# Performance work log

Hardware: AMD Instinct MI355X
Metric: run time of the kernel (lower is better)

## Reference

```python
import jax, jax.numpy as jnp
import numpy as np

T, B, I, H = 512, 64, 1024, 1024
DROPOUT = 0.3


def setup_inputs() -> dict:
    key = jax.random.key(0)
    k = jax.random.split(key, 6)
    s = 1.0 / np.sqrt(H).astype(np.float32)
    x = jax.random.normal(k[0], (T, B, I), dtype=jnp.float32)
    w_ih = jax.random.uniform(k[1], (4 * H, I), minval=-s, maxval=s, dtype=jnp.float32)
    w_hh = jax.random.uniform(k[2], (4 * H, H), minval=-s, maxval=s, dtype=jnp.float32)
    b_ih = jax.random.uniform(k[3], (4 * H,), minval=-s, maxval=s, dtype=jnp.float32)
    b_hh = jax.random.uniform(k[4], (4 * H,), minval=-s, maxval=s, dtype=jnp.float32)
    # init_weights: forget-gate bias (second quarter) set to 1
    b_ih = b_ih.at[H:2 * H].set(1.0)
    b_hh = b_hh.at[H:2 * H].set(1.0)
    # DropConnect mask on recurrent weights (training-mode dropout, fixed realization)
    keep = jax.random.bernoulli(k[5], 1.0 - DROPOUT, (4 * H, H))
    hh_mask = keep.astype(jnp.float32) / (1.0 - DROPOUT)
    return {"x": x, "w_ih": w_ih, "w_hh": w_hh, "b_ih": b_ih, "b_hh": b_hh, "hh_mask": hh_mask}


def reference(x, w_ih, w_hh, b_ih, b_hh, hh_mask):
    # x: (T, B, I). PyTorch LSTM gate order: i, f, g, o.
    h = w_hh.shape[1]
    w_hh_dropped = w_hh * hh_mask  # DropConnect applied once per forward
    # Precompute input contribution for all timesteps (one big GEMM): (T, B, 4H)
    gx = jnp.einsum('tbi,gi->tbg', x, w_ih) + b_ih + b_hh

    def step(carry, g_t):
        h_t, c_t = carry
        gates = g_t + h_t @ w_hh_dropped.T  # (B, 4H)
        i_g, f_g, g_g, o_g = jnp.split(gates, 4, axis=-1)
        i_g = jax.nn.sigmoid(i_g)
        f_g = jax.nn.sigmoid(f_g)
        g_g = jnp.tanh(g_g)
        o_g = jax.nn.sigmoid(o_g)
        c_new = f_g * c_t + i_g * g_g
        h_new = o_g * jnp.tanh(c_new)
        return (h_new, c_new), h_new

    bsz = x.shape[1]
    init = (jnp.zeros((bsz, h), x.dtype), jnp.zeros((bsz, h), x.dtype))
    (hn, cn), out = jax.lax.scan(step, init, gx)
    # match torch: output (T,B,H), hn/cn with leading num_layers dim
    return out, hn[None], cn[None]
```

## Files before the change

### kernel.cpp

```cpp
#include <hip/hip_runtime.h>

#define TT 512
#define BB 64
#define II 1024
#define HH 1024
#define GG 4096
#define BH 65536
#define NBLK 128

typedef __attribute__((ext_vector_type(8))) short bf16x8;
typedef __attribute__((ext_vector_type(4))) float f32x4;
typedef __attribute__((ext_vector_type(4))) unsigned u32x4;

__device__ __forceinline__ float bf2f(unsigned short u) {
  union { unsigned int i; float f; } v; v.i = ((unsigned int)u) << 16; return v.f;
}
__device__ __forceinline__ unsigned short f2bf(float f) {
  union { float f; unsigned int i; } v; v.f = f;
  return (unsigned short)((v.i + 0x7FFFu + ((v.i >> 16) & 1u)) >> 16);
}
__device__ __forceinline__ bf16x8 pack8(float4 a, float4 b) {
  union { bf16x8 v; unsigned short u[8]; } p;
  p.u[0] = f2bf(a.x); p.u[1] = f2bf(a.y); p.u[2] = f2bf(a.z); p.u[3] = f2bf(a.w);
  p.u[4] = f2bf(b.x); p.u[5] = f2bf(b.y); p.u[6] = f2bf(b.z); p.u[7] = f2bf(b.w);
  return p.v;
}
__device__ __forceinline__ float sigmoid_f(float x) { return 1.0f / (1.0f + __expf(-x)); }
__device__ __forceinline__ float tanh_f(float x) {
  float e = __expf(-2.0f * fabsf(x));
  float t = (1.0f - e) / (1.0f + e);
  return copysignf(t, x);
}

__device__ __forceinline__ void st32_uc(unsigned* p, unsigned v) {
  __hip_atomic_store(p, v, __ATOMIC_RELAXED, __HIP_MEMORY_SCOPE_AGENT);
}
__device__ __forceinline__ unsigned ld32_uc(const unsigned* p) {
  return __hip_atomic_load(p, __ATOMIC_RELAXED, __HIP_MEMORY_SCOPE_AGENT);
}
__device__ __forceinline__ void st128_uc(void* p, u32x4 v) {
  asm volatile("global_store_dwordx4 %0, %1, off sc0 sc1" :: "v"(p), "v"(v) : "memory");
}

__global__ __launch_bounds__(256) void wdlstm_xconv(
    const float* __restrict__ xc, unsigned short* __restrict__ xbf, int n4) {
  int stride = gridDim.x * blockDim.x;
  for (int i = blockIdx.x * blockDim.x + threadIdx.x; i < n4; i += stride) {
    float4 v = *(const float4*)(xc + (size_t)i * 4);
    unsigned short o[4] = {f2bf(v.x), f2bf(v.y), f2bf(v.z), f2bf(v.w)};
    *(unsigned long long*)(xbf + (size_t)i * 4) = *(unsigned long long*)o;
  }
}

__global__ __launch_bounds__(256) void wdlstm_fused(
    const float* __restrict__ w_hh, const float* __restrict__ hh_mask,
    const float* __restrict__ w_ih,
    const float* __restrict__ b_ih, const float* __restrict__ b_hh,
    const unsigned short* __restrict__ xbf,
    float* __restrict__ out, float* __restrict__ c_state,
    unsigned* __restrict__ flags,
    unsigned short* __restrict__ hinit,
    unsigned short* __restrict__ hring,
    int t0, int tc) {
  __shared__ __align__(16) char Wh[65536];
  __shared__ __align__(16) char Wi[65536];
  __shared__ float Dlds[64][35];
  __shared__ __align__(16) unsigned Hs[64][4];

  const int tid = threadIdx.x;
  const int wv  = tid >> 6, l = tid & 63;
  const int ln  = l & 15, lq = l >> 4;
  const int j0h = blockIdx.x * 8;
  unsigned* g_step = flags + 2048;

#pragma unroll
  for (int c8 = 0; c8 < 16; ++c8) {
    int c = tid + 256 * c8;
    int n = c >> 7, cc = c & 127;
    int wrow = (n >> 3) * HH + j0h + (n & 7);
    int addr = (n * 2048 + cc * 16) ^ ((n & 7) << 4);
    {
      const float* sw = w_hh   + (size_t)wrow * HH + cc * 8;
      const float* sm = hh_mask + (size_t)wrow * HH + cc * 8;
      float4 w0 = *(const float4*)sw, w1 = *(const float4*)(sw + 4);
      float4 m0 = *(const float4*)sm, m1 = *(const float4*)(sm + 4);
      float4 p0 = {w0.x * m0.x, w0.y * m0.y, w0.z * m0.z, w0.w * m0.w};
      float4 p1 = {w1.x * m1.x, w1.y * m1.y, w1.z * m1.z, w1.w * m1.w};
      *(bf16x8*)(Wh + addr) = pack8(p0, p1);
    }
    {
      const float* si = w_ih + (size_t)wrow * II + cc * 8;
      float4 a0 = *(const float4*)si, a1 = *(const float4*)(si + 4);
      *(bf16x8*)(Wi + addr) = pack8(a0, a1);
    }
  }
  __syncthreads();

  const int b_ep = l;
  const int jj0  = 2 * wv;
  float c_reg[2];
  if (t0 == 0) {
    c_reg[0] = c_reg[1] = 0.f;
  } else {
    float2 cv = *(const float2*)(c_state + (size_t)b_ep * HH + j0h + jj0);
    c_reg[0] = cv.x; c_reg[1] = cv.y;
  }
  float biasv[4][2];
#pragma unroll
  for (int g = 0; g < 4; ++g)
#pragma unroll
    for (int q = 0; q < 2; ++q) {
      int col = g * HH + j0h + jj0 + q;
      biasv[g][q] = b_ih[col] + b_hh[col];
    }

  float* hn_out = out + (size_t)TT * BH;
  float* cn_out = hn_out + BH;

  f32x4 gxacc[2];
  auto gx_compute = [&](int lt) {
    gxacc[0] = (f32x4){0.f, 0.f, 0.f, 0.f};
    gxacc[1] = (f32x4){0.f, 0.f, 0.f, 0.f};
    const unsigned short* ap = xbf + (size_t)lt * BH + (size_t)(16 * wv + ln) * II + lq * 8;
#pragma unroll 4
    for (int kc = 0; kc < 32; ++kc) {
      bf16x8 a = *(const bf16x8*)(ap + kc * 32);
#pragma unroll
      for (int ni = 0; ni < 2; ++ni) {
        int n = 16 * ni + ln;
        int baddr = (n * 2048 + kc * 64 + lq * 16) ^ ((n & 7) << 4);
        bf16x8 b = *(const bf16x8*)(Wi + baddr);
        gxacc[ni] = __builtin_amdgcn_mfma_f32_16x16x32_bf16(a, b, gxacc[ni], 0, 0, 0);
      }
    }
  };
  gx_compute(0);

  for (int lt = 0; lt < tc; ++lt) {
    const int t = t0 + lt;

    f32x4 acc[2] = {gxacc[0], gxacc[1]};

    if (t > 0) {
      if (blockIdx.x == 0) {
        if (tid < 64) {
          const unsigned* f0 = flags + (2 * tid) * 16;
          const unsigned* f1 = flags + (2 * tid + 1) * 16;
          while ((int)ld32_uc(f0) < t || (int)ld32_uc(f1) < t)
            __builtin_amdgcn_s_sleep(1);
          if (tid == 0) st32_uc(g_step, (unsigned)t);
        }
        __syncthreads();
      } else {
        if (tid == 0) {
          while ((int)ld32_uc(g_step) < t) __builtin_amdgcn_s_sleep(1);
        }
        __syncthreads();
      }

      const unsigned short* hp = (lt == 0) ? hinit
                                           : hring + (size_t)(lt - 1) * BH;
      const unsigned short* ap = hp + (size_t)(16 * wv + ln) * HH + lq * 8;
#pragma unroll 4
      for (int kc = 0; kc < 32; ++kc) {
        bf16x8 a = *(const bf16x8*)(ap + kc * 32);
#pragma unroll
        for (int ni = 0; ni < 2; ++ni) {
          int n = 16 * ni + ln;
          int baddr = (n * 2048 + kc * 64 + lq * 16) ^ ((n & 7) << 4);
          bf16x8 b = *(const bf16x8*)(Wh + baddr);
          acc[ni] = __builtin_amdgcn_mfma_f32_16x16x32_bf16(a, b, acc[ni], 0, 0, 0);
        }
      }
    }
#pragma unroll
    for (int ni = 0; ni < 2; ++ni)
#pragma unroll
      for (int r = 0; r < 4; ++r)
        Dlds[16 * wv + 4 * lq + r][16 * ni + ln] = acc[ni][r];
    __syncthreads();

    float hq[2];
#pragma unroll
    for (int q = 0; q < 2; ++q) {
      float g0 = Dlds[b_ep][ 0 + jj0 + q] + biasv[0][q];
      float g1 = Dlds[b_ep][ 8 + jj0 + q] + biasv[1][q];
      float g2 = Dlds[b_ep][16 + jj0 + q] + biasv[2][q];
      float g3 = Dlds[b_ep][24 + jj0 + q] + biasv[3][q];
      float ig = sigmoid_f(g0);
      float fg = sigmoid_f(g1);
      float gg = tanh_f(g2);
      float og = sigmoid_f(g3);
      c_reg[q] = fg * c_reg[q] + ig * gg;
      hq[q] = og * tanh_f(c_reg[q]);
    }
    *(float2*)(out + (size_t)t * BH + (size_t)b_ep * HH + j0h + jj0) = make_float2(hq[0], hq[1]);
    Hs[b_ep][wv] = (unsigned)f2bf(hq[0]) | ((unsigned)f2bf(hq[1]) << 16);
    if (t == TT - 1) {
      *(float2*)(hn_out + (size_t)b_ep * HH + j0h + jj0) = make_float2(hq[0], hq[1]);
      *(float2*)(cn_out + (size_t)b_ep * HH + j0h + jj0) = make_float2(c_reg[0], c_reg[1]);
    }

    __syncthreads();

    if (wv == 0) {
      u32x4 hv4 = *(const u32x4*)&Hs[l][0];
      char* dst = (char*)hring + ((size_t)lt * BH + (size_t)l * HH + j0h) * 2;
      st128_uc(dst, hv4);
      if (lt == tc - 1) {
        char* dsti = (char*)hinit + ((size_t)l * HH + j0h) * 2;
        st128_uc(dsti, hv4);
      }
      asm volatile("s_waitcnt vmcnt(0)" ::: "memory");
      if (tid == 0) st32_uc(&flags[blockIdx.x * 16], (unsigned)(t + 1));
    }

    if (lt + 1 < tc) gx_compute(lt + 1);
  }

  *(float2*)(c_state + (size_t)b_ep * HH + j0h + jj0) = make_float2(c_reg[0], c_reg[1]);
}

extern "C" void kernel_launch(void* const* d_in, const int* in_sizes, int n_in,
                              void* d_out, int out_size, void* d_ws, size_t ws_size,
                              hipStream_t stream) {
  const float* x       = (const float*)d_in[0];
  const float* w_ih    = (const float*)d_in[1];
  const float* w_hh    = (const float*)d_in[2];
  const float* b_ih    = (const float*)d_in[3];
  const float* b_hh    = (const float*)d_in[4];
  const float* hh_mask = (const float*)d_in[5];
  float* out           = (float*)d_out;

  char* ws = (char*)d_ws;
  float* c_state        = (float*)ws;
  unsigned* flags       = (unsigned*)(ws + 262144);
  unsigned short* hinit = (unsigned short*)(ws + 278528);
  unsigned short* hring = (unsigned short*)(ws + 409600);

  const long long fixed = 409600;
  const long long per_t = 131072 + 131072;
  long long avail = (long long)ws_size - fixed;
  int TC = (int)(avail / per_t);
  if (TC > 128) TC = 128;
  if (TC < 2) TC = 2;
  unsigned short* xbf = (unsigned short*)(ws + 409600 + (size_t)TC * 131072);

  hipMemsetAsync(flags, 0, 16384, stream);

  for (int t0 = 0; t0 < TT; t0 += TC) {
    int tc = TT - t0 < TC ? TT - t0 : TC;
    const float* xc = x + (size_t)t0 * BB * II;
    wdlstm_xconv<<<256, 256, 0, stream>>>(xc, xbf, tc * BH / 4);
    wdlstm_fused<<<NBLK, 256, 0, stream>>>(w_hh, hh_mask, w_ih, b_ih, b_hh, xbf,
                                           out, c_state, flags, hinit, hring, t0, tc);
  }
}
```

Baseline: 4.663 ms.

## Split recurrent K-reduction across two wave groups with 512-thread blocks

Doubles the block to 512 threads and splits each per-step GEMM's K dimension in half across two wave groups. The partial sums are reduced through a doubled LDS staging buffer, and the pointwise epilogue is reassigned so each thread owns one hidden column. All A-operand loads are also issued up front into registers before the MFMA chain, to hide global latency on the serial recurrent path. This shortens the per-step critical path, at the cost of more register pressure from the 16 preloaded vectors, an extra LDS add, and 8 waves contending for the CU.

New measurement: 4.585 ms. About the same (-1.7%).

```diff
diff --git a/kernel.cpp b/kernel.cpp
--- a/kernel.cpp
+++ b/kernel.cpp
@@ -52,7 +52,7 @@
   }
 }
 
-__global__ __launch_bounds__(256) void wdlstm_fused(
+__global__ __launch_bounds__(512) void wdlstm_fused(
     const float* __restrict__ w_hh, const float* __restrict__ hh_mask,
     const float* __restrict__ w_ih,
     const float* __restrict__ b_ih, const float* __restrict__ b_hh,
@@ -64,18 +64,20 @@
     int t0, int tc) {
   __shared__ __align__(16) char Wh[65536];
   __shared__ __align__(16) char Wi[65536];
-  __shared__ float Dlds[64][35];
-  __shared__ __align__(16) unsigned Hs[64][4];
+  __shared__ float Dlds[2][64][35];
+  __shared__ __align__(16) unsigned short Hs[64][8];
 
   const int tid = threadIdx.x;
   const int wv  = tid >> 6, l = tid & 63;
   const int ln  = l & 15, lq = l >> 4;
+  const int r0  = 16 * (wv & 3);
+  const int kh  = wv >> 2;
   const int j0h = blockIdx.x * 8;
   unsigned* g_step = flags + 2048;
 
 #pragma unroll
-  for (int c8 = 0; c8 < 16; ++c8) {
-    int c = tid + 256 * c8;
+  for (int c8 = 0; c8 < 8; ++c8) {
+    int c = tid + 512 * c8;
     int n = c >> 7, cc = c & 127;
     int wrow = (n >> 3) * HH + j0h + (n & 7);
     int addr = (n * 2048 + cc * 16) ^ ((n & 7) << 4);
@@ -96,23 +98,17 @@
   }
   __syncthreads();
 
-  const int b_ep = l;
-  const int jj0  = 2 * wv;
-  float c_reg[2];
-  if (t0 == 0) {
-    c_reg[0] = c_reg[1] = 0.f;
-  } else {
-    float2 cv = *(const float2*)(c_state + (size_t)b_ep * HH + j0h + jj0);
-    c_reg[0] = cv.x; c_reg[1] = cv.y;
-  }
-  float biasv[4][2];
-#pragma unroll
-  for (int g = 0; g < 4; ++g)
-#pragma unroll
-    for (int q = 0; q < 2; ++q) {
-      int col = g * HH + j0h + jj0 + q;
-      biasv[g][q] = b_ih[col] + b_hh[col];
-    }
+  const int b_ep = tid & 63;
+  const int jc   = tid >> 6;
+  float c_reg;
+  if (t0 == 0) c_reg = 0.f;
+  else         c_reg = c_state[(size_t)b_ep * HH + j0h + jc];
+  float biasv[4];
+#pragma unroll
+  for (int g = 0; g < 4; ++g) {
+    int col = g * HH + j0h + jc;
+    biasv[g] = b_ih[col] + b_hh[col];
+  }
 
   float* hn_out = out + (size_t)TT * BH;
   float* cn_out = hn_out + BH;
@@ -121,16 +117,19 @@
   auto gx_compute = [&](int lt) {
     gxacc[0] = (f32x4){0.f, 0.f, 0.f, 0.f};
     gxacc[1] = (f32x4){0.f, 0.f, 0.f, 0.f};
-    const unsigned short* ap = xbf + (size_t)lt * BH + (size_t)(16 * wv + ln) * II + lq * 8;
-#pragma unroll 4
-    for (int kc = 0; kc < 32; ++kc) {
-      bf16x8 a = *(const bf16x8*)(ap + kc * 32);
+    const unsigned short* ap = xbf + (size_t)lt * BH + (size_t)(r0 + ln) * II + kh * 512 + lq * 8;
+    bf16x8 areg[16];
+#pragma unroll
+    for (int i = 0; i < 16; ++i) areg[i] = *(const bf16x8*)(ap + i * 32);
+#pragma unroll
+    for (int i = 0; i < 16; ++i) {
+      int kb = kh * 1024 + i * 64;
 #pragma unroll
       for (int ni = 0; ni < 2; ++ni) {
         int n = 16 * ni + ln;
-        int baddr = (n * 2048 + kc * 64 + lq * 16) ^ ((n & 7) << 4);
+        int baddr = (n * 2048 + kb + lq * 16) ^ ((n & 7) << 4);
         bf16x8 b = *(const bf16x8*)(Wi + baddr);
-        gxacc[ni] = __builtin_amdgcn_mfma_f32_16x16x32_bf16(a, b, gxacc[ni], 0, 0, 0);
+        gxacc[ni] = __builtin_amdgcn_mfma_f32_16x16x32_bf16(areg[i], b, gxacc[ni], 0, 0, 0);
       }
     }
   };
@@ -160,16 +159,19 @@
 
       const unsigned short* hp = (lt == 0) ? hinit
                                            : hring + (size_t)(lt - 1) * BH;
-      const unsigned short* ap = hp + (size_t)(16 * wv + ln) * HH + lq * 8;
-#pragma unroll 4
-      for (int kc = 0; kc < 32; ++kc) {
-        bf16x8 a = *(const bf16x8*)(ap + kc * 32);
+      const unsigned short* ap = hp + (size_t)(r0 + ln) * HH + kh * 512 + lq * 8;
+      bf16x8 areg[16];
+#pragma unroll
+      for (int i = 0; i < 16; ++i) areg[i] = *(const bf16x8*)(ap + i * 32);
+#pragma unroll
+      for (int i = 0; i < 16; ++i) {
+        int kb = kh * 1024 + i * 64;
 #pragma unroll
         for (int ni = 0; ni < 2; ++ni) {
           int n = 16 * ni + ln;
-          int baddr = (n * 2048 + kc * 64 + lq * 16) ^ ((n & 7) << 4);
+          int baddr = (n * 2048 + kb + lq * 16) ^ ((n & 7) << 4);
           bf16x8 b = *(const bf16x8*)(Wh + baddr);
-          acc[ni] = __builtin_amdgcn_mfma_f32_16x16x32_bf16(a, b, acc[ni], 0, 0, 0);
+          acc[ni] = __builtin_amdgcn_mfma_f32_16x16x32_bf16(areg[i], b, acc[ni], 0, 0, 0);
         }
       }
     }
@@ -177,28 +179,24 @@
     for (int ni = 0; ni < 2; ++ni)
 #pragma unroll
       for (int r = 0; r < 4; ++r)
-        Dlds[16 * wv + 4 * lq + r][16 * ni + ln] = acc[ni][r];
+        Dlds[kh][r0 + 4 * lq + r][16 * ni + ln] = acc[ni][r];
     __syncthreads();
 
-    float hq[2];
-#pragma unroll
-    for (int q = 0; q < 2; ++q) {
-      float g0 = Dlds[b_ep][ 0 + jj0 + q] + biasv[0][q];
-      float g1 = Dlds[b_ep][ 8 + jj0 + q] + biasv[1][q];
-      float g2 = Dlds[b_ep][16 + jj0 + q] + biasv[2][q];
-      float g3 = Dlds[b_ep][24 + jj0 + q] + biasv[3][q];
-      float ig = sigmoid_f(g0);
-      float fg = sigmoid_f(g1);
-      float gg = tanh_f(g2);
-      float og = sigmoid_f(g3);
-      c_reg[q] = fg * c_reg[q] + ig * gg;
-      hq[q] = og * tanh_f(c_reg[q]);
-    }
-    *(float2*)(out + (size_t)t * BH + (size_t)b_ep * HH + j0h + jj0) = make_float2(hq[0], hq[1]);
-    Hs[b_ep][wv] = (unsigned)f2bf(hq[0]) | ((unsigned)f2bf(hq[1]) << 16);
+    float g0 = Dlds[0][b_ep][ 0 + jc] + Dlds[1][b_ep][ 0 + jc] + biasv[0];
+    float g1 = Dlds[0][b_ep][ 8 + jc] + Dlds[1][b_ep][ 8 + jc] + biasv[1];
+    float g2 = Dlds[0][b_ep][16 + jc] + Dlds[1][b_ep][16 + jc] + biasv[2];
+    float g3 = Dlds[0][b_ep][24 + jc] + Dlds[1][b_ep][24 + jc] + biasv[3];
+    float ig = sigmoid_f(g0);
+    float fg = sigmoid_f(g1);
+    float gg = tanh_f(g2);
+    float og = sigmoid_f(g3);
+    c_reg = fg * c_reg + ig * gg;
+    float h = og * tanh_f(c_reg);
+    out[(size_t)t * BH + (size_t)b_ep * HH + j0h + jc] = h;
+    Hs[b_ep][jc] = f2bf(h);
     if (t == TT - 1) {
-      *(float2*)(hn_out + (size_t)b_ep * HH + j0h + jj0) = make_float2(hq[0], hq[1]);
-      *(float2*)(cn_out + (size_t)b_ep * HH + j0h + jj0) = make_float2(c_reg[0], c_reg[1]);
+      hn_out[(size_t)b_ep * HH + j0h + jc] = h;
+      cn_out[(size_t)b_ep * HH + j0h + jc] = c_reg;
     }
 
     __syncthreads();
@@ -218,7 +216,7 @@
     if (lt + 1 < tc) gx_compute(lt + 1);
   }
 
-  *(float2*)(c_state + (size_t)b_ep * HH + j0h + jj0) = make_float2(c_reg[0], c_reg[1]);
+  c_state[(size_t)b_ep * HH + j0h + jc] = c_reg;
 }
 
 extern "C" void kernel_launch(void* const* d_in, const int* in_sizes, int n_in,
@@ -252,7 +250,7 @@
     int tc = TT - t0 < TC ? TT - t0 : TC;
     const float* xc = x + (size_t)t0 * BB * II;
     wdlstm_xconv<<<256, 256, 0, stream>>>(xc, xbf, tc * BH / 4);
-    wdlstm_fused<<<NBLK, 256, 0, stream>>>(w_hh, hh_mask, w_ih, b_ih, b_hh, xbf,
+    wdlstm_fused<<<NBLK, 512, 0, stream>>>(w_hh, hh_mask, w_ih, b_ih, b_hh, xbf,
                                            out, c_state, flags, hinit, hring, t0, tc);
   }
 }
```

## Warp-specialize LSTM kernel: separate recurrent, input-projection and grid-sync waves

Applied to the files above, without the earlier changes.

Splits each block into 9 waves. Four compute the recurrent matmul and cell update, four precompute input-projection gates up to four steps ahead into an LDS ring (stored as bf16), and one wave in block 0 acts as a dedicated grid-barrier coordinator. Block-wide __syncthreads calls are replaced with LDS atomic counters, and the A operands are double-buffered in registers. The aim is to take the input GEMM and barrier polling off the serial recurrent critical path. In exchange, the gx values are rounded to bf16 and the hand-rolled LDS synchronisation is more complex and riskier.

Result: slower. 4.824 ms (+3.4%).

```diff
diff --git a/kernel.cpp b/kernel.cpp
--- a/kernel.cpp
+++ b/kernel.cpp
@@ -40,6 +40,15 @@
 }
 __device__ __forceinline__ void st128_uc(void* p, u32x4 v) {
   asm volatile("global_store_dwordx4 %0, %1, off sc0 sc1" :: "v"(p), "v"(v) : "memory");
+}
+__device__ __forceinline__ void lds_add_rel(int* p) {
+  __hip_atomic_fetch_add(p, 1, __ATOMIC_RELEASE, __HIP_MEMORY_SCOPE_WORKGROUP);
+}
+__device__ __forceinline__ int lds_ld_acq(const int* p) {
+  return __hip_atomic_load(p, __ATOMIC_ACQUIRE, __HIP_MEMORY_SCOPE_WORKGROUP);
+}
+__device__ __forceinline__ void lds_st_rel(int* p, int v) {
+  __hip_atomic_store(p, v, __ATOMIC_RELEASE, __HIP_MEMORY_SCOPE_WORKGROUP);
 }
 
 __global__ __launch_bounds__(256) void wdlstm_xconv(
@@ -52,7 +61,7 @@
   }
 }
 
-__global__ __launch_bounds__(256) void wdlstm_fused(
+__global__ __launch_bounds__(576) void wdlstm_fused(
     const float* __restrict__ w_hh, const float* __restrict__ hh_mask,
     const float* __restrict__ w_ih,
     const float* __restrict__ b_ih, const float* __restrict__ b_hh,
@@ -64,8 +73,10 @@
     int t0, int tc) {
   __shared__ __align__(16) char Wh[65536];
   __shared__ __align__(16) char Wi[65536];
-  __shared__ float Dlds[64][35];
+  __shared__ float Dlds[64][33];
+  __shared__ __align__(8) unsigned short Dgx[4][32][72];
   __shared__ __align__(16) unsigned Hs[64][4];
+  __shared__ int syncv[8];
 
   const int tid = threadIdx.x;
   const int wv  = tid >> 6, l = tid & 63;
@@ -73,9 +84,7 @@
   const int j0h = blockIdx.x * 8;
   unsigned* g_step = flags + 2048;
 
-#pragma unroll
-  for (int c8 = 0; c8 < 16; ++c8) {
-    int c = tid + 256 * c8;
+  for (int c = tid; c < 4096; c += 576) {
     int n = c >> 7, cc = c & 127;
     int wrow = (n >> 3) * HH + j0h + (n & 7);
     int addr = (n * 2048 + cc * 16) ^ ((n & 7) << 4);
@@ -94,131 +103,171 @@
       *(bf16x8*)(Wi + addr) = pack8(a0, a1);
     }
   }
+  if (tid < 8) syncv[tid] = 0;
   __syncthreads();
 
-  const int b_ep = l;
-  const int jj0  = 2 * wv;
-  float c_reg[2];
-  if (t0 == 0) {
-    c_reg[0] = c_reg[1] = 0.f;
-  } else {
-    float2 cv = *(const float2*)(c_state + (size_t)b_ep * HH + j0h + jj0);
-    c_reg[0] = cv.x; c_reg[1] = cv.y;
+  if (wv < 4) {
+    const int b_ep = l;
+    const int jj0  = 2 * wv;
+    float c_reg[2];
+    if (t0 == 0) { c_reg[0] = c_reg[1] = 0.f; }
+    else {
+      float2 cv = *(const float2*)(c_state + (size_t)b_ep * HH + j0h + jj0);
+      c_reg[0] = cv.x; c_reg[1] = cv.y;
+    }
+    float biasv[4][2];
+#pragma unroll
+    for (int g = 0; g < 4; ++g)
+#pragma unroll
+      for (int q = 0; q < 2; ++q) {
+        int col = g * HH + j0h + jj0 + q;
+        biasv[g][q] = b_ih[col] + b_hh[col];
+      }
+    float* hn_out = out + (size_t)TT * BH;
+    float* cn_out = hn_out + BH;
+
+    for (int lt = 0; lt < tc; ++lt) {
+      const int t = t0 + lt;
+      f32x4 acc[2];
+      acc[0] = (f32x4){0.f, 0.f, 0.f, 0.f};
+      acc[1] = (f32x4){0.f, 0.f, 0.f, 0.f};
+
+      if (t > 0) {
+        while ((int)ld32_uc(g_step) < t) __builtin_amdgcn_s_sleep(1);
+        const unsigned short* hp = (lt == 0) ? hinit : hring + (size_t)(lt - 1) * BH;
+        const unsigned short* ap = hp + (size_t)(16 * wv + ln) * HH + lq * 8;
+        bf16x8 aA[8], aB[8];
+#pragma unroll
+        for (int i = 0; i < 8; ++i) aA[i] = *(const bf16x8*)(ap + i * 32);
+#pragma unroll
+        for (int c4 = 0; c4 < 4; ++c4) {
+          const bf16x8* cur = (c4 & 1) ? aB : aA;
+          bf16x8*       nxt = (c4 & 1) ? aA : aB;
+          if (c4 < 3) {
+#pragma unroll
+            for (int i = 0; i < 8; ++i) nxt[i] = *(const bf16x8*)(ap + (c4 + 1) * 256 + i * 32);
+          }
+#pragma unroll
+          for (int i = 0; i < 8; ++i) {
+            int kc = c4 * 8 + i;
+#pragma unroll
+            for (int ni = 0; ni < 2; ++ni) {
+              int n = 16 * ni + ln;
+              int baddr = (n * 2048 + kc * 64 + lq * 16) ^ ((n & 7) << 4);
+              bf16x8 b = *(const bf16x8*)(Wh + baddr);
+              acc[ni] = __builtin_amdgcn_mfma_f32_16x16x32_bf16(cur[i], b, acc[ni], 0, 0, 0);
+            }
+          }
+        }
+      }
+#pragma unroll
+      for (int ni = 0; ni < 2; ++ni)
+#pragma unroll
+        for (int r = 0; r < 4; ++r)
+          Dlds[16 * wv + 4 * lq + r][16 * ni + ln] = acc[ni][r];
+      if (l == 0) lds_add_rel(&syncv[0]);
+      {
+        const int tgt = 4 * (lt + 1);
+        while (lds_ld_acq(&syncv[0]) < tgt) __builtin_amdgcn_s_sleep(1);
+        while (lds_ld_acq(&syncv[2]) < lt + 1 || lds_ld_acq(&syncv[3]) < lt + 1 ||
+               lds_ld_acq(&syncv[4]) < lt + 1 || lds_ld_acq(&syncv[5]) < lt + 1)
+          __builtin_amdgcn_s_sleep(1);
+      }
+
+      const int slot = lt & 3;
+      float hq[2];
+#pragma unroll
+      for (int q = 0; q < 2; ++q) {
+        int jj = jj0 + q;
+        float g0 = Dlds[b_ep][ 0 + jj] + bf2f(Dgx[slot][ 0 + jj][b_ep]) + biasv[0][q];
+        float g1 = Dlds[b_ep][ 8 + jj] + bf2f(Dgx[slot][ 8 + jj][b_ep]) + biasv[1][q];
+        float g2 = Dlds[b_ep][16 + jj] + bf2f(Dgx[slot][16 + jj][b_ep]) + biasv[2][q];
+        float g3 = Dlds[b_ep][24 + jj] + bf2f(Dgx[slot][24 + jj][b_ep]) + biasv[3][q];
+        float ig = sigmoid_f(g0);
+        float fg = sigmoid_f(g1);
+        float gg = tanh_f(g2);
+        float og = sigmoid_f(g3);
+        c_reg[q] = fg * c_reg[q] + ig * gg;
+        hq[q] = og * tanh_f(c_reg[q]);
+      }
+      *(float2*)(out + (size_t)t * BH + (size_t)b_ep * HH + j0h + jj0) = make_float2(hq[0], hq[1]);
+      Hs[b_ep][wv] = (unsigned)f2bf(hq[0]) | ((unsigned)f2bf(hq[1]) << 16);
+      if (t == TT - 1) {
+        *(float2*)(hn_out + (size_t)b_ep * HH + j0h + jj0) = make_float2(hq[0], hq[1]);
+        *(float2*)(cn_out + (size_t)b_ep * HH + j0h + jj0) = make_float2(c_reg[0], c_reg[1]);
+      }
+      if (l == 0) lds_add_rel(&syncv[1]);
+
+      if (wv == 0) {
+        const int tgt = 4 * (lt + 1);
+        while (lds_ld_acq(&syncv[1]) < tgt) __builtin_amdgcn_s_sleep(1);
+        u32x4 hv4 = *(const u32x4*)&Hs[l][0];
+        char* dst = (char*)hring + ((size_t)lt * BH + (size_t)l * HH + j0h) * 2;
+        st128_uc(dst, hv4);
+        if (lt == tc - 1) {
+          char* dsti = (char*)hinit + ((size_t)l * HH + j0h) * 2;
+          st128_uc(dsti, hv4);
+        }
+        asm volatile("s_waitcnt vmcnt(0)" ::: "memory");
+        if (l == 0) st32_uc(&flags[blockIdx.x * 16], (unsigned)(t + 1));
+      }
+    }
+    *(float2*)(c_state + (size_t)b_ep * HH + j0h + jj0) = make_float2(c_reg[0], c_reg[1]);
+
+  } else if (wv < 8) {
+    const int w2 = wv - 4;
+    for (int s = 0; s < tc; ++s) {
+      if (s >= 4) {
+        const int tgt = 4 * (s - 3);
+        while (lds_ld_acq(&syncv[1]) < tgt) __builtin_amdgcn_s_sleep(1);
+      }
+      f32x4 acc[2];
+      acc[0] = (f32x4){0.f, 0.f, 0.f, 0.f};
+      acc[1] = (f32x4){0.f, 0.f, 0.f, 0.f};
+      const unsigned short* ap = xbf + (size_t)s * BH + (size_t)(16 * w2 + ln) * II + lq * 8;
+      bf16x8 aA[8], aB[8];
+#pragma unroll
+      for (int i = 0; i < 8; ++i) aA[i] = *(const bf16x8*)(ap + i * 32);
+#pragma unroll
+      for (int c4 = 0; c4 < 4; ++c4) {
+        const bf16x8* cur = (c4 & 1) ? aB : aA;
+        bf16x8*       nxt = (c4 & 1) ? aA : aB;
+        if (c4 < 3) {
+#pragma unroll
+          for (int i = 0; i < 8; ++i) nxt[i] = *(const bf16x8*)(ap + (c4 + 1) * 256 + i * 32);
+        }
+#pragma unroll
+        for (int i = 0; i < 8; ++i) {
+          int kc = c4 * 8 + i;
+#pragma unroll
+          for (int ni = 0; ni < 2; ++ni) {
+            int n = 16 * ni + ln;
+            int baddr = (n * 2048 + kc * 64 + lq * 16) ^ ((n & 7) << 4);
+            bf16x8 b = *(const bf16x8*)(Wi + baddr);
+            acc[ni] = __builtin_amdgcn_mfma_f32_16x16x32_bf16(cur[i], b, acc[ni], 0, 0, 0);
+          }
+        }
+      }
+      const int slot = s & 3;
+#pragma unroll
+      for (int ni = 0; ni < 2; ++ni) {
+        unsigned short p[4] = {f2bf(acc[ni][0]), f2bf(acc[ni][1]),
+                               f2bf(acc[ni][2]), f2bf(acc[ni][3])};
+        *(unsigned long long*)&Dgx[slot][16 * ni + ln][16 * w2 + 4 * lq] =
+            *(unsigned long long*)p;
+      }
+      if (l == 0) lds_st_rel(&syncv[2 + w2], s + 1);
+    }
+
+  } else if (blockIdx.x == 0) {
+    const unsigned* f0 = flags + (2 * l) * 16;
+    const unsigned* f1 = flags + (2 * l + 1) * 16;
+    for (int s = t0; s < t0 + tc; ++s) {
+      while ((int)ld32_uc(f0) < s || (int)ld32_uc(f1) < s)
+        __builtin_amdgcn_s_sleep(1);
+      if (l == 0) st32_uc(g_step, (unsigned)s);
+    }
   }
-  float biasv[4][2];
-#pragma unroll
-  for (int g = 0; g < 4; ++g)
-#pragma unroll
-    for (int q = 0; q < 2; ++q) {
-      int col = g * HH + j0h + jj0 + q;
-      biasv[g][q] = b_ih[col] + b_hh[col];
-    }
-
-  float* hn_out = out + (size_t)TT * BH;
-  float* cn_out = hn_out + BH;
-
-  f32x4 gxacc[2];
-  auto gx_compute = [&](int lt) {
-    gxacc[0] = (f32x4){0.f, 0.f, 0.f, 0.f};
-    gxacc[1] = (f32x4){0.f, 0.f, 0.f, 0.f};
-    const unsigned short* ap = xbf + (size_t)lt * BH + (size_t)(16 * wv + ln) * II + lq * 8;
-#pragma unroll 4
-    for (int kc = 0; kc < 32; ++kc) {
-      bf16x8 a = *(const bf16x8*)(ap + kc * 32);
-#pragma unroll
-      for (int ni = 0; ni < 2; ++ni) {
-        int n = 16 * ni + ln;
-        int baddr = (n * 2048 + kc * 64 + lq * 16) ^ ((n & 7) << 4);
-        bf16x8 b = *(const bf16x8*)(Wi + baddr);
-        gxacc[ni] = __builtin_amdgcn_mfma_f32_16x16x32_bf16(a, b, gxacc[ni], 0, 0, 0);
-      }
-    }
-  };
-  gx_compute(0);
-
-  for (int lt = 0; lt < tc; ++lt) {
-    const int t = t0 + lt;
-
-    f32x4 acc[2] = {gxacc[0], gxacc[1]};
-
-    if (t > 0) {
-      if (blockIdx.x == 0) {
-        if (tid < 64) {
-          const unsigned* f0 = flags + (2 * tid) * 16;
-          const unsigned* f1 = flags + (2 * tid + 1) * 16;
-          while ((int)ld32_uc(f0) < t || (int)ld32_uc(f1) < t)
-            __builtin_amdgcn_s_sleep(1);
-          if (tid == 0) st32_uc(g_step, (unsigned)t);
-        }
-        __syncthreads();
-      } else {
-        if (tid == 0) {
-          while ((int)ld32_uc(g_step) < t) __builtin_amdgcn_s_sleep(1);
-        }
-        __syncthreads();
-      }
-
-      const unsigned short* hp = (lt == 0) ? hinit
-                                           : hring + (size_t)(lt - 1) * BH;
-      const unsigned short* ap = hp + (size_t)(16 * wv + ln) * HH + lq * 8;
-#pragma unroll 4
-      for (int kc = 0; kc < 32; ++kc) {
-        bf16x8 a = *(const bf16x8*)(ap + kc * 32);
-#pragma unroll
-        for (int ni = 0; ni < 2; ++ni) {
-          int n = 16 * ni + ln;
-          int baddr = (n * 2048 + kc * 64 + lq * 16) ^ ((n & 7) << 4);
-          bf16x8 b = *(const bf16x8*)(Wh + baddr);
-          acc[ni] = __builtin_amdgcn_mfma_f32_16x16x32_bf16(a, b, acc[ni], 0, 0, 0);
-        }
-      }
-    }
-#pragma unroll
-    for (int ni = 0; ni < 2; ++ni)
-#pragma unroll
-      for (int r = 0; r < 4; ++r)
-        Dlds[16 * wv + 4 * lq + r][16 * ni + ln] = acc[ni][r];
-    __syncthreads();
-
-    float hq[2];
-#pragma unroll
-    for (int q = 0; q < 2; ++q) {
-      float g0 = Dlds[b_ep][ 0 + jj0 + q] + biasv[0][q];
-      float g1 = Dlds[b_ep][ 8 + jj0 + q] + biasv[1][q];
-      float g2 = Dlds[b_ep][16 + jj0 + q] + biasv[2][q];
-      float g3 = Dlds[b_ep][24 + jj0 + q] + biasv[3][q];
-      float ig = sigmoid_f(g0);
-      float fg = sigmoid_f(g1);
-      float gg = tanh_f(g2);
-      float og = sigmoid_f(g3);
-      c_reg[q] = fg * c_reg[q] + ig * gg;
-      hq[q] = og * tanh_f(c_reg[q]);
-    }
-    *(float2*)(out + (size_t)t * BH + (size_t)b_ep * HH + j0h + jj0) = make_float2(hq[0], hq[1]);
-    Hs[b_ep][wv] = (unsigned)f2bf(hq[0]) | ((unsigned)f2bf(hq[1]) << 16);
-    if (t == TT - 1) {
-      *(float2*)(hn_out + (size_t)b_ep * HH + j0h + jj0) = make_float2(hq[0], hq[1]);
-      *(float2*)(cn_out + (size_t)b_ep * HH + j0h + jj0) = make_float2(c_reg[0], c_reg[1]);
-    }
-
-    __syncthreads();
-
-    if (wv == 0) {
-      u32x4 hv4 = *(const u32x4*)&Hs[l][0];
-      char* dst = (char*)hring + ((size_t)lt * BH + (size_t)l * HH + j0h) * 2;
-      st128_uc(dst, hv4);
-      if (lt == tc - 1) {
-        char* dsti = (char*)hinit + ((size_t)l * HH + j0h) * 2;
-        st128_uc(dsti, hv4);
-      }
-      asm volatile("s_waitcnt vmcnt(0)" ::: "memory");
-      if (tid == 0) st32_uc(&flags[blockIdx.x * 16], (unsigned)(t + 1));
-    }
-
-    if (lt + 1 < tc) gx_compute(lt + 1);
-  }
-
-  *(float2*)(c_state + (size_t)b_ep * HH + j0h + jj0) = make_float2(c_reg[0], c_reg[1]);
 }
 
 extern "C" void kernel_launch(void* const* d_in, const int* in_sizes, int n_in,
@@ -252,7 +301,7 @@
     int tc = TT - t0 < TC ? TT - t0 : TC;
     const float* xc = x + (size_t)t0 * BB * II;
     wdlstm_xconv<<<256, 256, 0, stream>>>(xc, xbf, tc * BH / 4);
-    wdlstm_fused<<<NBLK, 256, 0, stream>>>(w_hh, hh_mask, w_ih, b_ih, b_hh, xbf,
+    wdlstm_fused<<<NBLK, 576, 0, stream>>>(w_hh, hh_mask, w_ih, b_ih, b_hh, xbf,
                                            out, c_state, flags, hinit, hring, t0, tc);
   }
 }
```
